# Performance work log

Hardware: AMD Instinct MI355X
Metric: run time of the kernel (lower is better)

## Reference

```python
import jax, jax.numpy as jnp
import numpy as np

TAU = 20.0
TH = 1.0
TAU_THETA = 50.0
THETA_INC = 0.5
REFRAC_STEPS = 5
K = 10.0  # surrogate sigmoid sharpness
B, L = 65536, 400


def setup_inputs() -> dict:
    key = jax.random.key(0)
    I = jax.random.normal(key, (B, L), dtype=jnp.float32)
    return {"I": I}


def _lif_forward(I):
    Bn, Ln = I.shape
    dt = I.dtype

    def step(carry, I_t):
        v, theta, ref = carry
        # Euler membrane update: v += -v/tau + I_t
        v = v + (-v / TAU + I_t)
        can_spike = (ref == 0)
        x = v - theta
        s_soft = jax.nn.sigmoid(K * x) * can_spike.astype(dt)
        s_hard = ((x >= 0.0) & can_spike).astype(dt)
        # straight-through: value = s_hard, gradient flows through s_soft
        s = jax.lax.stop_gradient(s_hard - s_soft) + s_soft
        ref = jnp.where(s_hard > 0, jnp.int32(REFRAC_STEPS), jnp.maximum(ref - 1, 0))
        # reset uses detached spike (multiplier is a constant wrt grad)
        v = v * (1.0 - jax.lax.stop_gradient(s))
        # adaptive threshold: decay to base + bump on hard spike
        theta = theta - (theta - TH) / TAU_THETA + THETA_INC * s_hard
        return (v, theta, ref), (s, s_hard)

    init = (jnp.zeros((Bn,), dt), jnp.full((Bn,), TH, dt), jnp.zeros((Bn,), jnp.int32))
    _, (spikes_t, hard_t) = jax.lax.scan(step, init, jnp.swapaxes(I, 0, 1))
    spikes = jnp.swapaxes(spikes_t, 0, 1)       # [B, L]
    hard_spikes = jnp.swapaxes(hard_t, 0, 1)    # [B, L]
    return spikes, hard_spikes


def _soft_lat(spikes):
    Ln = spikes.shape[1]
    time = jnp.arange(Ln, dtype=spikes.dtype)
    w = spikes / (spikes.sum(axis=1, keepdims=True) + 1e-6)
    return (w * time).sum(axis=1)


def reference(I):
    spikes, hard_spikes = _lif_forward(I)
    fired = hard_spikes > 0.5
    has_spike = jnp.any(fired, axis=1)
    first_idx = jnp.argmax(fired, axis=1)
    hard_latency = jnp.where(has_spike, first_idx, I.shape[1]).astype(jnp.int64)
    soft_latency = _soft_lat(spikes)
    return spikes, hard_latency, soft_latency
```

## Files before the change

kernel.cpp:

```cpp
#include <hip/hip_runtime.h>


constexpr int Bsz   = 65536;
constexpr int Lsz   = 400;
constexpr int ROWS  = 64;
constexpr int TC    = 40;
constexpr int NCH   = Lsz / TC;
constexpr int STRIDE = TC + 1;
constexpr int V4    = TC / 4;

__global__ __launch_bounds__(ROWS)
void lif_kernel(const float* __restrict__ I, float* __restrict__ out)
{
    __shared__ float tile[ROWS * STRIDE];

    const int tid = threadIdx.x;
    const int rb  = blockIdx.x * ROWS;
    const int row = rb + tid;

    const float* Irow = I   + (size_t)row * Lsz;
    float*       Sb   = out + (size_t)rb  * Lsz;

    float4 regA[V4], regB[V4];

    auto glb_load = [&](int ch, float4* rg) {
#pragma unroll
        for (int it = 0; it < V4; ++it)
            rg[it] = *reinterpret_cast<const float4*>(Irow + ch * TC + it * 4);
    };

    float v     = 0.0f;
    float theta = 1.0f;
    int   allow = 0;
    int   first = Lsz;
    float cnt   = 0.0f;
    float swt   = 0.0f;

    auto body = [&](int ch, const float4* rg) {
        float* myrow = &tile[tid * STRIDE];
        float cnt_l = 0.0f, swt_l = 0.0f;
        const int t0 = ch * TC;

        auto step = [&](float It, int c) {
            const int t = t0 + c;
            v = __builtin_fmaf(v, 0.95f, It);
            const bool hard = (v >= theta) & (t >= allow);
            const float s   = hard ? 1.0f : 0.0f;
            v     = hard ? 0.0f : v;
            theta = __builtin_fmaf(theta, 0.98f, hard ? 0.52f : 0.02f);
            allow = hard ? (t + 6) : allow;
            myrow[c] = s;
            cnt_l += s;
            swt_l = __builtin_fmaf(s, (float)c, swt_l);
            first = hard ? min(first, t) : first;
        };

#pragma unroll
        for (int c4 = 0; c4 < V4; ++c4) {
            const float4 q = rg[c4];
            step(q.x, c4 * 4 + 0);
            step(q.y, c4 * 4 + 1);
            step(q.z, c4 * 4 + 2);
            step(q.w, c4 * 4 + 3);
        }
        swt = __builtin_fmaf(cnt_l, (float)t0, swt + swt_l);
        cnt += cnt_l;
    };

    auto store = [&](int ch) {
        const int t0 = ch * TC;
#pragma unroll
        for (int it = 0; it < V4; ++it) {
            const int idx = it * ROWS + tid;
            const int r   = idx / V4;
            const int c4  = idx % V4;
            const float* sp = &tile[r * STRIDE + c4 * 4];
            const float4 vv = make_float4(sp[0], sp[1], sp[2], sp[3]);
            *reinterpret_cast<float4*>(Sb + r * Lsz + t0 + c4 * 4) = vv;
        }
    };

    glb_load(0, regA);
    glb_load(1, regB);

    for (int ch = 0; ch < NCH; ch += 2) {
        body(ch, regA);
        if (ch + 2 < NCH) glb_load(ch + 2, regA);
        store(ch);
        body(ch + 1, regB);
        if (ch + 3 < NCH) glb_load(ch + 3, regB);
        store(ch + 1);
    }

    out[(size_t)Bsz * Lsz + row]       = (float)first;
    out[(size_t)Bsz * Lsz + Bsz + row] = swt / (cnt + 1e-6f);
}

extern "C" void kernel_launch(void* const* d_in, const int* in_sizes, int n_in,
                              void* d_out, int out_size, void* d_ws, size_t ws_size,
                              hipStream_t stream)
{
    const float* I = (const float*)d_in[0];
    float* out = (float*)d_out;
    lif_kernel<<<dim3(Bsz / ROWS), dim3(ROWS), 0, stream>>>(I, out);
}
```

Baseline: 41.94 us.

## Pack spikes as bitmasks in LDS and expand in larger nontemporal store batches

Spikes are no longer written as floats into a padded shared tile. Each thread packs them into 32-bit bitmasks in registers, dumps those to a small LDS buffer, and expands them into float4 nontemporal stores covering 160 timesteps at a time (20 for the tail). This cuts LDS traffic and footprint and makes fewer, larger output write phases. In exchange it adds bit-manipulation ALU work, and the kernel has no explicit barriers between LDS writes and cross-thread reads, which rests on the one-wavefront block assumption.

Measured after the change: 53.74 us. +28.1%, slower.

```diff
diff --git a/kernel.cpp b/kernel.cpp
--- a/kernel.cpp
+++ b/kernel.cpp
@@ -1,18 +1,39 @@
 #include <hip/hip_runtime.h>
 
 
-constexpr int Bsz   = 65536;
-constexpr int Lsz   = 400;
-constexpr int ROWS  = 64;
-constexpr int TC    = 40;
-constexpr int NCH   = Lsz / TC;
-constexpr int STRIDE = TC + 1;
-constexpr int V4    = TC / 4;
+constexpr int Bsz  = 65536;
+constexpr int Lsz  = 400;
+constexpr int ROWS = 64;
+constexpr int TC   = 40;
+constexpr int V4   = TC / 4;
+
+typedef float floatx4 __attribute__((ext_vector_type(4)));
+
+template<int CNT4>
+__device__ __forceinline__ void expand(const unsigned int* bits_lds, float* Sb,
+                                       int tid, int t0f)
+{
+#pragma unroll
+    for (int it = 0; it < CNT4; ++it) {
+        const int idx = it * ROWS + tid;
+        const int r   = idx / CNT4;
+        const int c4  = idx % CNT4;
+        const unsigned int word = bits_lds[r * 8 + (c4 >> 3)];
+        const int bb = (c4 & 7) * 4;
+        floatx4 vv;
+        vv.x = ((word >> (bb + 0)) & 1u) ? 1.0f : 0.0f;
+        vv.y = ((word >> (bb + 1)) & 1u) ? 1.0f : 0.0f;
+        vv.z = ((word >> (bb + 2)) & 1u) ? 1.0f : 0.0f;
+        vv.w = ((word >> (bb + 3)) & 1u) ? 1.0f : 0.0f;
+        __builtin_nontemporal_store(vv,
+            reinterpret_cast<floatx4*>(Sb + (size_t)r * Lsz + t0f + c4 * 4));
+    }
+}
 
 __global__ __launch_bounds__(ROWS)
 void lif_kernel(const float* __restrict__ I, float* __restrict__ out)
 {
-    __shared__ float tile[ROWS * STRIDE];
+    __shared__ unsigned int bits_lds[ROWS * 8];
 
     const int tid = threadIdx.x;
     const int rb  = blockIdx.x * ROWS;
@@ -35,62 +56,57 @@
     int   first = Lsz;
     float cnt   = 0.0f;
     float swt   = 0.0f;
+    unsigned int bw[5];
 
-    auto body = [&](int ch, const float4* rg) {
-        float* myrow = &tile[tid * STRIDE];
+    auto body = [&](const float4* rg, int t0, int gb) {
+        const float* in = reinterpret_cast<const float*>(rg);
         float cnt_l = 0.0f, swt_l = 0.0f;
-        const int t0 = ch * TC;
-
-        auto step = [&](float It, int c) {
+#pragma unroll
+        for (int c = 0; c < TC; ++c) {
+            const float It = in[c];
+            v = __builtin_fmaf(v, 0.95f, It);
             const int t = t0 + c;
-            v = __builtin_fmaf(v, 0.95f, It);
             const bool hard = (v >= theta) & (t >= allow);
-            const float s   = hard ? 1.0f : 0.0f;
             v     = hard ? 0.0f : v;
             theta = __builtin_fmaf(theta, 0.98f, hard ? 0.52f : 0.02f);
             allow = hard ? (t + 6) : allow;
-            myrow[c] = s;
+            const int cg = gb + c;
+            bw[cg >> 5] |= (hard ? (1u << (cg & 31)) : 0u);
+            const float s = hard ? 1.0f : 0.0f;
             cnt_l += s;
             swt_l = __builtin_fmaf(s, (float)c, swt_l);
             first = hard ? min(first, t) : first;
-        };
-
-#pragma unroll
-        for (int c4 = 0; c4 < V4; ++c4) {
-            const float4 q = rg[c4];
-            step(q.x, c4 * 4 + 0);
-            step(q.y, c4 * 4 + 1);
-            step(q.z, c4 * 4 + 2);
-            step(q.w, c4 * 4 + 3);
         }
         swt = __builtin_fmaf(cnt_l, (float)t0, swt + swt_l);
         cnt += cnt_l;
     };
 
-    auto store = [&](int ch) {
-        const int t0 = ch * TC;
-#pragma unroll
-        for (int it = 0; it < V4; ++it) {
-            const int idx = it * ROWS + tid;
-            const int r   = idx / V4;
-            const int c4  = idx % V4;
-            const float* sp = &tile[r * STRIDE + c4 * 4];
-            const float4 vv = make_float4(sp[0], sp[1], sp[2], sp[3]);
-            *reinterpret_cast<float4*>(Sb + r * Lsz + t0 + c4 * 4) = vv;
-        }
+    auto dump_bits = [&]() {
+        *reinterpret_cast<uint4*>(&bits_lds[tid * 8]) =
+            make_uint4(bw[0], bw[1], bw[2], bw[3]);
+        bits_lds[tid * 8 + 4] = bw[4];
     };
 
     glb_load(0, regA);
     glb_load(1, regB);
 
-    for (int ch = 0; ch < NCH; ch += 2) {
-        body(ch, regA);
-        if (ch + 2 < NCH) glb_load(ch + 2, regA);
-        store(ch);
-        body(ch + 1, regB);
-        if (ch + 3 < NCH) glb_load(ch + 3, regB);
-        store(ch + 1);
+    for (int g = 0; g < 2; ++g) {
+        bw[0] = bw[1] = bw[2] = bw[3] = bw[4] = 0u;
+#pragma unroll
+        for (int k = 0; k < 4; ++k) {
+            const int ch = g * 4 + k;
+            if ((k & 1) == 0) { body(regA, ch * TC, k * TC); glb_load(ch + 2, regA); }
+            else              { body(regB, ch * TC, k * TC); glb_load(ch + 2, regB); }
+        }
+        dump_bits();
+        expand<40>(bits_lds, Sb, tid, g * 160);
     }
+
+    bw[0] = bw[1] = bw[2] = bw[3] = bw[4] = 0u;
+    body(regA, 8 * TC, 0);
+    body(regB, 9 * TC, 40);
+    dump_bits();
+    expand<20>(bits_lds, Sb, tid, 320);
 
     out[(size_t)Bsz * Lsz + row]       = (float)first;
     out[(size_t)Bsz * Lsz + Bsz + row] = swt / (cnt + 1e-6f);
```

## Stream input chunks via async global-to-LDS loads with coalesced double buffering

Applied to the files above, without the earlier changes.

Input loading changes from per-row strided float4 loads into registers to coalesced global_load_lds DMA into a double-buffered shared-memory staging area. Each thread then reads its own row from LDS. The intent is better coalescing and lower register pressure while the next chunk arrives asynchronously. There is no explicit waitcnt or barrier between the async LDS writes and the reads, so correctness depends on compiler-inserted waits. The per-thread LDS reads use stride TC and may hit bank conflicts.

New measurement: 46.76 us. 11.5% more time.

```diff
diff --git a/kernel.cpp b/kernel.cpp
--- a/kernel.cpp
+++ b/kernel.cpp
@@ -1,32 +1,48 @@
 #include <hip/hip_runtime.h>
 
 
-constexpr int Bsz   = 65536;
-constexpr int Lsz   = 400;
-constexpr int ROWS  = 64;
-constexpr int TC    = 40;
-constexpr int NCH   = Lsz / TC;
+constexpr int Bsz  = 65536;
+constexpr int Lsz  = 400;
+constexpr int ROWS = 64;
+constexpr int TC   = 40;
+constexpr int NCH  = Lsz / TC;
 constexpr int STRIDE = TC + 1;
-constexpr int V4    = TC / 4;
+constexpr int V4   = TC / 4;
+
+__device__ __forceinline__ void gl2lds16(const float* g, float* l)
+{
+    __builtin_amdgcn_global_load_lds(
+        (const __attribute__((address_space(1))) void*)g,
+        (__attribute__((address_space(3))) void*)l,
+        16, 0, 0);
+}
 
 __global__ __launch_bounds__(ROWS)
 void lif_kernel(const float* __restrict__ I, float* __restrict__ out)
 {
+    __shared__ float inbuf[2][ROWS * TC];
     __shared__ float tile[ROWS * STRIDE];
 
     const int tid = threadIdx.x;
     const int rb  = blockIdx.x * ROWS;
     const int row = rb + tid;
 
-    const float* Irow = I   + (size_t)row * Lsz;
-    float*       Sb   = out + (size_t)rb  * Lsz;
+    const float* Ib = I   + (size_t)rb * Lsz;
+    float*       Sb = out + (size_t)rb * Lsz;
 
-    float4 regA[V4], regB[V4];
+    int goff[V4];
+#pragma unroll
+    for (int k = 0; k < V4; ++k) {
+        const int idx = k * ROWS + tid;
+        const int r   = idx / V4;
+        const int c4  = idx % V4;
+        goff[k] = r * Lsz + c4 * 4;
+    }
 
-    auto glb_load = [&](int ch, float4* rg) {
+    auto issue = [&](int ch, float* buf) {
 #pragma unroll
-        for (int it = 0; it < V4; ++it)
-            rg[it] = *reinterpret_cast<const float4*>(Irow + ch * TC + it * 4);
+        for (int k = 0; k < V4; ++k)
+            gl2lds16(Ib + goff[k] + ch * TC, buf + k * 256);
     };
 
     float v     = 0.0f;
@@ -35,15 +51,18 @@
     int   first = Lsz;
     float cnt   = 0.0f;
     float swt   = 0.0f;
+    float4 rg[V4];
 
-    auto body = [&](int ch, const float4* rg) {
+    auto body = [&](int ch) {
         float* myrow = &tile[tid * STRIDE];
+        const float* in = reinterpret_cast<const float*>(rg);
         float cnt_l = 0.0f, swt_l = 0.0f;
         const int t0 = ch * TC;
-
-        auto step = [&](float It, int c) {
+#pragma unroll
+        for (int c = 0; c < TC; ++c) {
+            const float It = in[c];
+            v = __builtin_fmaf(v, 0.95f, It);
             const int t = t0 + c;
-            v = __builtin_fmaf(v, 0.95f, It);
             const bool hard = (v >= theta) & (t >= allow);
             const float s   = hard ? 1.0f : 0.0f;
             v     = hard ? 0.0f : v;
@@ -53,15 +72,6 @@
             cnt_l += s;
             swt_l = __builtin_fmaf(s, (float)c, swt_l);
             first = hard ? min(first, t) : first;
-        };
-
-#pragma unroll
-        for (int c4 = 0; c4 < V4; ++c4) {
-            const float4 q = rg[c4];
-            step(q.x, c4 * 4 + 0);
-            step(q.y, c4 * 4 + 1);
-            step(q.z, c4 * 4 + 2);
-            step(q.w, c4 * 4 + 3);
         }
         swt = __builtin_fmaf(cnt_l, (float)t0, swt + swt_l);
         cnt += cnt_l;
@@ -80,16 +90,17 @@
         }
     };
 
-    glb_load(0, regA);
-    glb_load(1, regB);
+    issue(0, inbuf[0]);
+    issue(1, inbuf[1]);
 
-    for (int ch = 0; ch < NCH; ch += 2) {
-        body(ch, regA);
-        if (ch + 2 < NCH) glb_load(ch + 2, regA);
+    for (int ch = 0; ch < NCH; ++ch) {
+        float* buf = inbuf[ch & 1];
+#pragma unroll
+        for (int j = 0; j < V4; ++j)
+            rg[j] = *reinterpret_cast<const float4*>(&buf[tid * TC + j * 4]);
+        body(ch);
+        if (ch + 2 < NCH) issue(ch + 2, buf);
         store(ch);
-        body(ch + 1, regB);
-        if (ch + 3 < NCH) glb_load(ch + 3, regB);
-        store(ch + 1);
     }
 
     out[(size_t)Bsz * Lsz + row]       = (float)first;
```
